# Optimization experiments

Hardware: AMD Instinct MI355X
Metric: run time of the kernel (lower is better)

The kernel has to match this reference:

```python
import jax, jax.numpy as jnp
import numpy as np

B, S, D, O, H, E, K = 4, 1024, 1024, 1024, 2048, 8, 2
EPS = 1e-5

def _layernorm(x, g, b):
    m = jnp.mean(x, axis=-1, keepdims=True)
    v = jnp.mean(jnp.square(x - m), axis=-1, keepdims=True)
    return (x - m) * jax.lax.rsqrt(v + EPS) * g + b

def setup_inputs() -> dict:
    key = jax.random.key(0)
    ks = jax.random.split(key, 8)
    def xavier(k, shape):
        fan_out, fan_in = shape[-2], shape[-1]
        bound = float(np.sqrt(6.0 / (fan_in + fan_out)))
        return jax.random.uniform(k, shape, jnp.float32, -bound, bound)
    return {
        "x": jax.random.normal(ks[0], (B, S, D), jnp.float32),
        "ln1_g": jnp.ones((D,), jnp.float32), "ln1_b": jnp.zeros((D,), jnp.float32),
        "router_w": xavier(ks[1], (E, D)), "router_b": jnp.zeros((E,), jnp.float32),
        "sh_w1": xavier(ks[2], (H, D)), "sh_b1": jnp.zeros((H,), jnp.float32),
        "sh_w2": xavier(ks[3], (O, H)), "sh_b2": jnp.zeros((O,), jnp.float32),
        "e_w1": xavier(ks[4], (E, H, D)), "e_b1": jnp.zeros((E, H), jnp.float32),
        "e_w2": xavier(ks[5], (E, O, H)), "e_b2": jnp.zeros((E, O), jnp.float32),
        "ln2_g": jnp.ones((O,), jnp.float32), "ln2_b": jnp.zeros((O,), jnp.float32),
    }

def reference(x, ln1_g, ln1_b, router_w, router_b, sh_w1, sh_b1, sh_w2, sh_b2,
              e_w1, e_b1, e_w2, e_b2, ln2_g, ln2_b):
    # eval mode: no router noise, no aux loss
    x_norm = _layernorm(x, ln1_g, ln1_b)               # [B,S,D]
    xf = x_norm.reshape(-1, D)                          # [T,D]
    logits = xf @ router_w.T + router_b                 # [T,E]
    probs = jax.nn.softmax(logits, axis=-1)
    tk_w, tk_i = jax.lax.top_k(probs, K)                # [T,K]
    tk_w = tk_w / jnp.sum(tk_w, axis=-1, keepdims=True)
    # shared expert (exact GELU, as torch nn.GELU default)
    shared = jax.nn.gelu(xf @ sh_w1.T + sh_b1, approximate=False) @ sh_w2.T + sh_b2  # [T,O]
    # all experts densely, combined sparsely by top-k weights
    hid = jax.nn.gelu(jnp.einsum('td,ehd->teh', xf, e_w1) + e_b1, approximate=False)  # [T,E,H]
    eout = jnp.einsum('teh,eoh->teo', hid, e_w2) + e_b2                                # [T,E,O]
    comb_w = jnp.sum(jax.nn.one_hot(tk_i, E, dtype=xf.dtype) * tk_w[..., None], axis=1)  # [T,E]
    out = shared * (1.0 / (E + 1)) + jnp.einsum('te,teo->to', comb_w, eout)           # [T,O]
    out = _layernorm(out.reshape(B, S, O), ln2_g, ln2_b)
    return out
```

## Files before the change

kernel.cpp:

```cpp
#include <hip/hip_runtime.h>
#include <math.h>
#include <stdint.h>

typedef unsigned short u16;
typedef unsigned int u32;

typedef __attribute__((ext_vector_type(8))) short bf16x8;
typedef __attribute__((ext_vector_type(4))) float f32x4;

#define ASYNC_COPY16(g, l)                                                         \
  __builtin_amdgcn_global_load_lds((__attribute__((address_space(1))) const void*)(g), \
                                   (__attribute__((address_space(3))) void*)(l), 16, 0, 0)

__device__ __forceinline__ float bf2f(u16 u) {
  union { u32 i; float f; } v; v.i = ((u32)u) << 16; return v.f;
}
__device__ __forceinline__ u16 f2bf(float f) {
  union { float f; u32 i; } v; v.f = f;
  u32 r = v.i + 0x7fffu + ((v.i >> 16) & 1u);
  return (u16)(r >> 16);
}
__device__ __forceinline__ float gelu_fast(float x) {
  float t = x * x;
  float z = 1.5957691f * x * (1.0f + 0.044715f * t);
  return x / (1.0f + __expf(-z));
}

__global__ __launch_bounds__(256) void cvt_all_k(
    const float* __restrict__ s0, const float* __restrict__ s1,
    const float* __restrict__ s2, const float* __restrict__ s3,
    u16* __restrict__ dst)
{
  const int64_t i0 = (int64_t)blockIdx.x * 2048 + (int64_t)threadIdx.x * 8;
  const float* src; int64_t rel;
  if (i0 < 2097152)       { src = s0; rel = i0; }
  else if (i0 < 4194304)  { src = s1; rel = i0 - 2097152; }
  else if (i0 < 20971520) { src = s2; rel = i0 - 4194304; }
  else                    { src = s3; rel = i0 - 20971520; }
  const float4 a = *(const float4*)(src + rel);
  const float4 b = *(const float4*)(src + rel + 4);
  union { u16 h[8]; uint4 v; } o;
  o.h[0] = f2bf(a.x); o.h[1] = f2bf(a.y); o.h[2] = f2bf(a.z); o.h[3] = f2bf(a.w);
  o.h[4] = f2bf(b.x); o.h[5] = f2bf(b.y); o.h[6] = f2bf(b.z); o.h[7] = f2bf(b.w);
  *(uint4*)(dst + i0) = o.v;
}

__global__ __launch_bounds__(256) void ln_router_k(
    const float* __restrict__ x, const float* __restrict__ g, const float* __restrict__ b,
    const float* __restrict__ rw, const float* __restrict__ rb,
    u16* __restrict__ xn, int* __restrict__ tk_idx, float* __restrict__ tk_w)
{
  const int t = blockIdx.x, tid = threadIdx.x;
  __shared__ float xs[1024];
  __shared__ float red[8];
  __shared__ float logits[8];
  const int wave = tid >> 6, lane = tid & 63;

  const float4 xv = *(const float4*)(x + (size_t)t * 1024 + 4 * tid);
  float v0 = xv.x, v1 = xv.y, v2 = xv.z, v3 = xv.w;
  float s = v0 + v1 + v2 + v3;
  float q = v0 * v0 + v1 * v1 + v2 * v2 + v3 * v3;
#pragma unroll
  for (int o = 32; o > 0; o >>= 1) { s += __shfl_down(s, o, 64); q += __shfl_down(q, o, 64); }
  if (lane == 0) { red[wave] = s; red[4 + wave] = q; }
  __syncthreads();
  if (tid == 0) {
    float S = red[0] + red[1] + red[2] + red[3];
    float Q = red[4] + red[5] + red[6] + red[7];
    float mean = S * (1.0f / 1024.0f);
    float var = Q * (1.0f / 1024.0f) - mean * mean;
    red[0] = mean; red[1] = rsqrtf(var + 1e-5f);
  }
  __syncthreads();
  const float mean = red[0], rstd = red[1];
  float vv[4] = {v0, v1, v2, v3};
  union { u16 h[4]; uint2 v; } pk;
#pragma unroll
  for (int j = 0; j < 4; ++j) {
    int d = 4 * tid + j;
    float y = (vv[j] - mean) * rstd * g[d] + b[d];
    xs[d] = y;
    pk.h[j] = f2bf(y);
  }
  *(uint2*)(xn + (size_t)t * 1024 + 4 * tid) = pk.v;
  __syncthreads();
#pragma unroll
  for (int pe = 0; pe < 2; ++pe) {
    int e = wave + 4 * pe;
    const float* wrow = rw + (size_t)e * 1024;
    float acc = 0.f;
#pragma unroll
    for (int j = 0; j < 16; ++j) {
      int d = lane + 64 * j;
      acc += xs[d] * wrow[d];
    }
#pragma unroll
    for (int o = 32; o > 0; o >>= 1) acc += __shfl_down(acc, o, 64);
    if (lane == 0) logits[e] = acc + rb[e];
  }
  __syncthreads();
  if (tid == 0) {
    int i0 = 0; float l0 = logits[0];
#pragma unroll
    for (int e = 1; e < 8; ++e) if (logits[e] > l0) { l0 = logits[e]; i0 = e; }
    int i1 = -1; float l1 = -3.4e38f;
#pragma unroll
    for (int e = 0; e < 8; ++e) { if (e == i0) continue; if (logits[e] > l1) { l1 = logits[e]; i1 = e; } }
    float w0 = 1.0f / (1.0f + expf(l1 - l0));
    float w1 = 1.0f - w0;
    tk_idx[2 * t] = i0; tk_idx[2 * t + 1] = i1;
    tk_w[2 * t] = w0; tk_w[2 * t + 1] = w1;
  }
}

__device__ __forceinline__ uint4 u4_add(uint4 a, uint4 b) {
  uint4 r; r.x = a.x + b.x; r.y = a.y + b.y; r.z = a.z + b.z; r.w = a.w + b.w; return r;
}
__device__ __forceinline__ uint4 u4_sub(uint4 a, uint4 b) {
  uint4 r; r.x = a.x - b.x; r.y = a.y - b.y; r.z = a.z - b.z; r.w = a.w - b.w; return r;
}

__global__ __launch_bounds__(256) void assign_k(
    const int* __restrict__ tk_idx, const float* __restrict__ tk_w,
    int* __restrict__ offs, int* __restrict__ slot_token,
    float* __restrict__ slot_w, int* __restrict__ slot_of)
{
  const int tid = threadIdx.x, lane = tid & 63, wave = tid >> 6;
  int eidx[32];
#pragma unroll
  for (int j = 0; j < 32; ++j) eidx[j] = tk_idx[tid * 32 + j];

  uint4 p = {0u, 0u, 0u, 0u};
#pragma unroll
  for (int j = 0; j < 32; ++j) {
    int e = eidx[j];
    unsigned inc = 1u << ((e & 1) * 16);
    int c = e >> 1;
    if (c == 0) p.x += inc; else if (c == 1) p.y += inc;
    else if (c == 2) p.z += inc; else p.w += inc;
  }
  const uint4 own = p;
#pragma unroll
  for (int o = 1; o < 64; o <<= 1) {
    uint4 t;
    t.x = (u32)__shfl_up((int)p.x, o, 64);
    t.y = (u32)__shfl_up((int)p.y, o, 64);
    t.z = (u32)__shfl_up((int)p.z, o, 64);
    t.w = (u32)__shfl_up((int)p.w, o, 64);
    if (lane >= o) p = u4_add(p, t);
  }
  __shared__ uint4 wtot[4];
  __shared__ int offs_s[9];
  if (lane == 63) wtot[wave] = p;
  __syncthreads();
  uint4 wbase = {0u, 0u, 0u, 0u};
  uint4 gtot = {0u, 0u, 0u, 0u};
#pragma unroll
  for (int w2 = 0; w2 < 4; ++w2) {
    uint4 t = wtot[w2];
    if (w2 < wave) wbase = u4_add(wbase, t);
    gtot = u4_add(gtot, t);
  }
  const uint4 excl = u4_sub(p, own);
  if (tid == 0) {
    int gtots[8] = { (int)(gtot.x & 0xffff), (int)(gtot.x >> 16),
                     (int)(gtot.y & 0xffff), (int)(gtot.y >> 16),
                     (int)(gtot.z & 0xffff), (int)(gtot.z >> 16),
                     (int)(gtot.w & 0xffff), (int)(gtot.w >> 16) };
    int a = 0;
#pragma unroll
    for (int e = 0; e < 8; ++e) { offs_s[e] = a; offs[e] = a; a += gtots[e]; }
    offs_s[8] = a; offs[8] = a;
  }
  __syncthreads();
  const uint4 pre = u4_add(wbase, excl);
  int base[8];
  base[0] = offs_s[0] + (int)(pre.x & 0xffff);
  base[1] = offs_s[1] + (int)(pre.x >> 16);
  base[2] = offs_s[2] + (int)(pre.y & 0xffff);
  base[3] = offs_s[3] + (int)(pre.y >> 16);
  base[4] = offs_s[4] + (int)(pre.z & 0xffff);
  base[5] = offs_s[5] + (int)(pre.z >> 16);
  base[6] = offs_s[6] + (int)(pre.w & 0xffff);
  base[7] = offs_s[7] + (int)(pre.w >> 16);
#pragma unroll
  for (int j = 0; j < 32; ++j) {
    int idx = tid * 32 + j;
    int e = eidx[j];
    int s = base[e]++;
    slot_token[s] = idx >> 1;
    slot_w[s] = tk_w[idx];
    slot_of[idx] = s;
  }
}

template <int N, int KD, int STAGE>
__global__ __launch_bounds__(256) void gemm_fused_k(
    const u16* __restrict__ Abase, const u16* __restrict__ Bsh,
    const u16* __restrict__ Bex, const float* __restrict__ bias_sh,
    const float* __restrict__ bias_ex,
    u16* __restrict__ outH,
    const int* __restrict__ offs, const int* __restrict__ slot_token,
    const float* __restrict__ slot_w)
{
  const int tid = threadIdx.x;
  const int z = blockIdx.z;
  int off = 0, cnt = 4096, obase = 0;
  const u16* B = Bsh;
  const float* biasp = bias_sh;
  if (z > 0) {
    off = offs[z - 1]; cnt = offs[z] - off; obase = 4096 + off;
    B = Bex + (size_t)(z - 1) * N * KD;
    biasp = bias_ex + (size_t)(z - 1) * N;
  }
  const int m0 = blockIdx.y * 128;
  if (m0 >= cnt) return;
  const int n0 = blockIdx.x * 128;

  __shared__ u16 lA[2][4096];
  __shared__ u16 lB[2][4096];

  const int rS = tid >> 2;
  const int c8 = (tid & 3) * 8;

  int ra0 = m0 + rS;      if (ra0 > cnt - 1) ra0 = cnt - 1;
  int ra1 = m0 + rS + 64; if (ra1 > cnt - 1) ra1 = cnt - 1;
  size_t arow0, arow1;
  if (STAGE == 1) {
    if (z == 0) { arow0 = (size_t)ra0; arow1 = (size_t)ra1; }
    else        { arow0 = (size_t)slot_token[off + ra0]; arow1 = (size_t)slot_token[off + ra1]; }
  } else {
    if (z == 0) { arow0 = (size_t)ra0; arow1 = (size_t)ra1; }
    else        { arow0 = (size_t)(4096 + off + ra0); arow1 = (size_t)(4096 + off + ra1); }
  }
  const u16* gA0 = Abase + arow0 * KD + c8;
  const u16* gA1 = Abase + arow1 * KD + c8;
  const u16* gB0 = B + (size_t)(n0 + rS) * KD + c8;
  const u16* gB1 = B + (size_t)(n0 + rS + 64) * KD + c8;

  const int wave = tid >> 6, lane = tid & 63;
  const int wr = wave >> 1, wc = wave & 1;
  const int fr = lane & 15, fq = lane >> 4;

  f32x4 acc[4][4];
  const f32x4 zero = {0.f, 0.f, 0.f, 0.f};
#pragma unroll
  for (int i = 0; i < 4; ++i)
#pragma unroll
    for (int n = 0; n < 4; ++n) acc[i][n] = zero;

  const int NK = KD / 32;
  {
    ASYNC_COPY16(gA0, &lA[0][0] + wave * 512);
    ASYNC_COPY16(gA1, &lA[0][0] + 2048 + wave * 512);
    ASYNC_COPY16(gB0, &lB[0][0] + wave * 512);
    ASYNC_COPY16(gB1, &lB[0][0] + 2048 + wave * 512);
    gA0 += 32; gA1 += 32; gB0 += 32; gB1 += 32;
  }

  for (int kb = 0; kb < NK; ++kb) {
    const int cur = kb & 1;
    __syncthreads();
    if (kb + 1 < NK) {
      ASYNC_COPY16(gA0, &lA[cur ^ 1][0] + wave * 512);
      ASYNC_COPY16(gA1, &lA[cur ^ 1][0] + 2048 + wave * 512);
      ASYNC_COPY16(gB0, &lB[cur ^ 1][0] + wave * 512);
      ASYNC_COPY16(gB1, &lB[cur ^ 1][0] + 2048 + wave * 512);
      gA0 += 32; gA1 += 32; gB0 += 32; gB1 += 32;
    }
    const u16* rdA = &lA[cur][0] + (wr * 64 + fr) * 32 + fq * 8;
    const u16* rdB = &lB[cur][0] + (wc * 64 + fr) * 32 + fq * 8;
    bf16x8 af[4], bfv[4];
#pragma unroll
    for (int i = 0; i < 4; ++i) af[i] = *(const bf16x8*)(rdA + i * 16 * 32);
#pragma unroll
    for (int n = 0; n < 4; ++n) bfv[n] = *(const bf16x8*)(rdB + n * 16 * 32);
#pragma unroll
    for (int i = 0; i < 4; ++i)
#pragma unroll
      for (int n = 0; n < 4; ++n)
        acc[i][n] = __builtin_amdgcn_mfma_f32_16x16x32_bf16(af[i], bfv[n], acc[i][n], 0, 0, 0);
  }

  const int colBase = n0 + wc * 64;
#pragma unroll
  for (int i = 0; i < 4; ++i) {
    const int mlBase = m0 + wr * 64 + i * 16 + fq * 4;
#pragma unroll
    for (int r = 0; r < 4; ++r) {
      const int ml = mlBase + r;
      if (ml >= cnt) continue;
      const size_t orow = (size_t)(obase + ml) * N;
      float rwgt = (STAGE == 2) ? ((z == 0) ? (1.0f / 9.0f) : slot_w[off + ml]) : 1.f;
#pragma unroll
      for (int n = 0; n < 4; ++n) {
        const int col = colBase + n * 16 + fr;
        float v = acc[i][n][r] + biasp[col];
        if (STAGE == 1) v = gelu_fast(v);
        else            v = v * rwgt;
        outH[orow + col] = f2bf(v);
      }
    }
  }
}

__global__ __launch_bounds__(256) void combine_ln2_k(
    const u16* __restrict__ sh_out, const u16* __restrict__ eout,
    const int* __restrict__ slot_of,
    const float* __restrict__ g2, const float* __restrict__ b2,
    float* __restrict__ out)
{
  const int t = blockIdx.x, tid = threadIdx.x;
  const int wave = tid >> 6, lane = tid & 63;
  __shared__ float red[8];
  const size_t s0 = (size_t)slot_of[2 * t], s1 = (size_t)slot_of[2 * t + 1];
  union { uint2 v; u16 h[4]; } a, c0, c1;
  a.v  = *(const uint2*)(sh_out + (size_t)t * 1024 + 4 * tid);
  c0.v = *(const uint2*)(eout + s0 * 1024 + 4 * tid);
  c1.v = *(const uint2*)(eout + s1 * 1024 + 4 * tid);
  float vv[4];
#pragma unroll
  for (int j = 0; j < 4; ++j) vv[j] = bf2f(a.h[j]) + bf2f(c0.h[j]) + bf2f(c1.h[j]);
  float s = vv[0] + vv[1] + vv[2] + vv[3];
  float q = vv[0] * vv[0] + vv[1] * vv[1] + vv[2] * vv[2] + vv[3] * vv[3];
#pragma unroll
  for (int o = 32; o > 0; o >>= 1) { s += __shfl_down(s, o, 64); q += __shfl_down(q, o, 64); }
  if (lane == 0) { red[wave] = s; red[4 + wave] = q; }
  __syncthreads();
  if (tid == 0) {
    float S = red[0] + red[1] + red[2] + red[3];
    float Q = red[4] + red[5] + red[6] + red[7];
    float mean = S * (1.0f / 1024.0f);
    float var = Q * (1.0f / 1024.0f) - mean * mean;
    red[0] = mean; red[1] = rsqrtf(var + 1e-5f);
  }
  __syncthreads();
  const float mean = red[0], rstd = red[1];
#pragma unroll
  for (int j = 0; j < 4; ++j) {
    int d = 4 * tid + j;
    out[(size_t)t * 1024 + d] = (vv[j] - mean) * rstd * g2[d] + b2[d];
  }
}

extern "C" void kernel_launch(void* const* d_in, const int* in_sizes, int n_in,
                              void* d_out, int out_size, void* d_ws, size_t ws_size,
                              hipStream_t stream)
{
  const float* x     = (const float*)d_in[0];
  const float* ln1_g = (const float*)d_in[1];
  const float* ln1_b = (const float*)d_in[2];
  const float* rw    = (const float*)d_in[3];
  const float* rb    = (const float*)d_in[4];
  const float* sh_w1 = (const float*)d_in[5];
  const float* sh_b1 = (const float*)d_in[6];
  const float* sh_w2 = (const float*)d_in[7];
  const float* sh_b2 = (const float*)d_in[8];
  const float* e_w1  = (const float*)d_in[9];
  const float* e_b1  = (const float*)d_in[10];
  const float* e_w2  = (const float*)d_in[11];
  const float* e_b2  = (const float*)d_in[12];
  const float* ln2_g = (const float*)d_in[13];
  const float* ln2_b = (const float*)d_in[14];
  float* out = (float*)d_out;

  char* w = (char*)d_ws;
  u16*   x_norm = (u16*)(w + 0);
  u16*   hid    = (u16*)(w + (8u << 20));
  u16*   outb   = (u16*)(w + (56u << 20));
  u16*   w1b    = (u16*)(w + (104u << 20));
  u16*   w2b    = (u16*)(w + (108u << 20));
  u16*   ew1b   = (u16*)(w + (112u << 20));
  u16*   ew2b   = (u16*)(w + (144u << 20));
  char*  meta   = w + (176u << 20);
  int*   tk_idx     = (int*)(meta);
  float* tk_w       = (float*)(meta + (32u << 10));
  int*   slot_token = (int*)(meta + (64u << 10));
  float* slot_w     = (float*)(meta + (96u << 10));
  int*   slot_of    = (int*)(meta + (128u << 10));
  int*   offs       = (int*)(meta + (160u << 10));

  cvt_all_k<<<18432, 256, 0, stream>>>(sh_w1, sh_w2, e_w1, e_w2, w1b);

  ln_router_k<<<4096, 256, 0, stream>>>(x, ln1_g, ln1_b, rw, rb, x_norm, tk_idx, tk_w);
  assign_k<<<1, 256, 0, stream>>>(tk_idx, tk_w, offs, slot_token, slot_w, slot_of);

  gemm_fused_k<2048, 1024, 1><<<dim3(16, 32, 9), 256, 0, stream>>>(
      x_norm, w1b, ew1b, sh_b1, e_b1, hid, offs, slot_token, nullptr);
  gemm_fused_k<1024, 2048, 2><<<dim3(8, 32, 9), 256, 0, stream>>>(
      hid, w2b, ew2b, sh_b2, e_b2, outb, offs, slot_token, slot_w);

  combine_ln2_k<<<4096, 256, 0, stream>>>(outb, outb + (size_t)4096 * 1024,
                                          slot_of, ln2_g, ln2_b, out);
}
```

Before: 438.6 us.

## Use one wave per token in LN kernels and swizzle GEMM tile order

The LN1+router and combine+LN2 kernels now assign one wave per token with four tokens per block. This removes the block-wide __syncthreads reductions and lets the code use vectorized float4 gamma/beta and router-weight loads. The GEMM kernels remap blockIdx into grouped M/N tiles so that neighbouring blocks share A and B panels in cache. The early-exit check for empty expert tiles now depends on the remapped m0, and the router uses the faster __expf.

```diff
diff --git a/kernel.cpp b/kernel.cpp
--- a/kernel.cpp
+++ b/kernel.cpp
@@ -50,66 +50,69 @@
     const float* __restrict__ rw, const float* __restrict__ rb,
     u16* __restrict__ xn, int* __restrict__ tk_idx, float* __restrict__ tk_w)
 {
-  const int t = blockIdx.x, tid = threadIdx.x;
-  __shared__ float xs[1024];
-  __shared__ float red[8];
-  __shared__ float logits[8];
-  const int wave = tid >> 6, lane = tid & 63;
-
-  const float4 xv = *(const float4*)(x + (size_t)t * 1024 + 4 * tid);
-  float v0 = xv.x, v1 = xv.y, v2 = xv.z, v3 = xv.w;
-  float s = v0 + v1 + v2 + v3;
-  float q = v0 * v0 + v1 * v1 + v2 * v2 + v3 * v3;
+  __shared__ float xs[4][1024];
+  const int wave = threadIdx.x >> 6, lane = threadIdx.x & 63;
+  const int t = blockIdx.x * 4 + wave;
+
+  const float* xrow = x + (size_t)t * 1024;
+  float4 v[4];
+#pragma unroll
+  for (int j = 0; j < 4; ++j) v[j] = *(const float4*)(xrow + lane * 4 + j * 256);
+  float s = 0.f, q = 0.f;
+#pragma unroll
+  for (int j = 0; j < 4; ++j) {
+    s += v[j].x + v[j].y + v[j].z + v[j].w;
+    q += v[j].x * v[j].x + v[j].y * v[j].y + v[j].z * v[j].z + v[j].w * v[j].w;
+  }
 #pragma unroll
   for (int o = 32; o > 0; o >>= 1) { s += __shfl_down(s, o, 64); q += __shfl_down(q, o, 64); }
-  if (lane == 0) { red[wave] = s; red[4 + wave] = q; }
-  __syncthreads();
-  if (tid == 0) {
-    float S = red[0] + red[1] + red[2] + red[3];
-    float Q = red[4] + red[5] + red[6] + red[7];
-    float mean = S * (1.0f / 1024.0f);
-    float var = Q * (1.0f / 1024.0f) - mean * mean;
-    red[0] = mean; red[1] = rsqrtf(var + 1e-5f);
-  }
-  __syncthreads();
-  const float mean = red[0], rstd = red[1];
-  float vv[4] = {v0, v1, v2, v3};
-  union { u16 h[4]; uint2 v; } pk;
+  s = __shfl(s, 0, 64); q = __shfl(q, 0, 64);
+  const float mean = s * (1.0f / 1024.0f);
+  const float rstd = rsqrtf(q * (1.0f / 1024.0f) - mean * mean + 1e-5f);
+
 #pragma unroll
   for (int j = 0; j < 4; ++j) {
-    int d = 4 * tid + j;
-    float y = (vv[j] - mean) * rstd * g[d] + b[d];
-    xs[d] = y;
-    pk.h[j] = f2bf(y);
-  }
-  *(uint2*)(xn + (size_t)t * 1024 + 4 * tid) = pk.v;
-  __syncthreads();
-#pragma unroll
-  for (int pe = 0; pe < 2; ++pe) {
-    int e = wave + 4 * pe;
-    const float* wrow = rw + (size_t)e * 1024;
-    float acc = 0.f;
-#pragma unroll
-    for (int j = 0; j < 16; ++j) {
-      int d = lane + 64 * j;
-      acc += xs[d] * wrow[d];
-    }
-#pragma unroll
-    for (int o = 32; o > 0; o >>= 1) acc += __shfl_down(acc, o, 64);
-    if (lane == 0) logits[e] = acc + rb[e];
-  }
-  __syncthreads();
-  if (tid == 0) {
-    int i0 = 0; float l0 = logits[0];
-#pragma unroll
-    for (int e = 1; e < 8; ++e) if (logits[e] > l0) { l0 = logits[e]; i0 = e; }
+    const int d0 = lane * 4 + j * 256;
+    const float4 gv = *(const float4*)(g + d0);
+    const float4 bv = *(const float4*)(b + d0);
+    float y0 = (v[j].x - mean) * rstd * gv.x + bv.x;
+    float y1 = (v[j].y - mean) * rstd * gv.y + bv.y;
+    float y2 = (v[j].z - mean) * rstd * gv.z + bv.z;
+    float y3 = (v[j].w - mean) * rstd * gv.w + bv.w;
+    float4 yv = {y0, y1, y2, y3};
+    *(float4*)(&xs[wave][d0]) = yv;
+    union { u16 h[4]; uint2 u; } pk;
+    pk.h[0] = f2bf(y0); pk.h[1] = f2bf(y1); pk.h[2] = f2bf(y2); pk.h[3] = f2bf(y3);
+    *(uint2*)(xn + (size_t)t * 1024 + d0) = pk.u;
+  }
+
+  const int e = lane >> 3, c = lane & 7;
+  const float* wrow = rw + (size_t)e * 1024;
+  float acc = 0.f;
+#pragma unroll
+  for (int i = 0; i < 32; ++i) {
+    const int d4 = 4 * (c + 8 * i);
+    const float4 wv = *(const float4*)(wrow + d4);
+    const float4 xv = *(const float4*)(&xs[wave][d4]);
+    acc += xv.x * wv.x + xv.y * wv.y + xv.z * wv.z + xv.w * wv.w;
+  }
+  acc += __shfl_xor(acc, 1, 64);
+  acc += __shfl_xor(acc, 2, 64);
+  acc += __shfl_xor(acc, 4, 64);
+  const float logit = acc + rb[e];
+  float l[8];
+#pragma unroll
+  for (int ee = 0; ee < 8; ++ee) l[ee] = __shfl(logit, ee * 8, 64);
+  if (lane == 0) {
+    int i0 = 0; float l0 = l[0];
+#pragma unroll
+    for (int k = 1; k < 8; ++k) if (l[k] > l0) { l0 = l[k]; i0 = k; }
     int i1 = -1; float l1 = -3.4e38f;
 #pragma unroll
-    for (int e = 0; e < 8; ++e) { if (e == i0) continue; if (logits[e] > l1) { l1 = logits[e]; i1 = e; } }
-    float w0 = 1.0f / (1.0f + expf(l1 - l0));
-    float w1 = 1.0f - w0;
+    for (int k = 0; k < 8; ++k) { if (k == i0) continue; if (l[k] > l1) { l1 = l[k]; i1 = k; } }
+    float w0 = 1.0f / (1.0f + __expf(l1 - l0));
     tk_idx[2 * t] = i0; tk_idx[2 * t + 1] = i1;
-    tk_w[2 * t] = w0; tk_w[2 * t + 1] = w1;
+    tk_w[2 * t] = w0; tk_w[2 * t + 1] = 1.0f - w0;
   }
 }
 
@@ -195,7 +198,7 @@
 }
 
 template <int N, int KD, int STAGE>
-__global__ __launch_bounds__(256) void gemm_fused_k(
+__device__ __forceinline__ void gemm_body(
     const u16* __restrict__ Abase, const u16* __restrict__ Bsh,
     const u16* __restrict__ Bex, const float* __restrict__ bias_sh,
     const float* __restrict__ bias_ex,
@@ -213,9 +216,12 @@
     B = Bex + (size_t)(z - 1) * N * KD;
     biasp = bias_ex + (size_t)(z - 1) * N;
   }
-  const int m0 = blockIdx.y * 128;
+  constexpr int NT = N / 128;
+  const int bx = blockIdx.x, by = blockIdx.y;
+  const int r = bx & 7, sgl = bx >> 3;
+  const int m0 = (r + 8 * (by >> 3)) * 128;
   if (m0 >= cnt) return;
-  const int n0 = blockIdx.x * 128;
+  const int n0 = (sgl + (NT >> 3) * (by & 7)) * 128;
 
   __shared__ u16 lA[2][4096];
   __shared__ u16 lB[2][4096];
@@ -287,15 +293,15 @@
   for (int i = 0; i < 4; ++i) {
     const int mlBase = m0 + wr * 64 + i * 16 + fq * 4;
 #pragma unroll
-    for (int r = 0; r < 4; ++r) {
-      const int ml = mlBase + r;
+    for (int rr = 0; rr < 4; ++rr) {
+      const int ml = mlBase + rr;
       if (ml >= cnt) continue;
       const size_t orow = (size_t)(obase + ml) * N;
       float rwgt = (STAGE == 2) ? ((z == 0) ? (1.0f / 9.0f) : slot_w[off + ml]) : 1.f;
 #pragma unroll
       for (int n = 0; n < 4; ++n) {
         const int col = colBase + n * 16 + fr;
-        float v = acc[i][n][r] + biasp[col];
+        float v = acc[i][n][rr] + biasp[col];
         if (STAGE == 1) v = gelu_fast(v);
         else            v = v * rwgt;
         outH[orow + col] = f2bf(v);
@@ -304,42 +310,70 @@
   }
 }
 
+__global__ __launch_bounds__(256) void fc1_k(
+    const u16* __restrict__ Abase, const u16* __restrict__ Bsh,
+    const u16* __restrict__ Bex, const float* __restrict__ bias_sh,
+    const float* __restrict__ bias_ex, u16* __restrict__ outH,
+    const int* __restrict__ offs, const int* __restrict__ slot_token,
+    const float* __restrict__ slot_w)
+{
+  gemm_body<2048, 1024, 1>(Abase, Bsh, Bex, bias_sh, bias_ex, outH, offs, slot_token, slot_w);
+}
+
+__global__ __launch_bounds__(256) void fc2_k(
+    const u16* __restrict__ Abase, const u16* __restrict__ Bsh,
+    const u16* __restrict__ Bex, const float* __restrict__ bias_sh,
+    const float* __restrict__ bias_ex, u16* __restrict__ outH,
+    const int* __restrict__ offs, const int* __restrict__ slot_token,
+    const float* __restrict__ slot_w)
+{
+  gemm_body<1024, 2048, 2>(Abase, Bsh, Bex, bias_sh, bias_ex, outH, offs, slot_token, slot_w);
+}
+
 __global__ __launch_bounds__(256) void combine_ln2_k(
     const u16* __restrict__ sh_out, const u16* __restrict__ eout,
     const int* __restrict__ slot_of,
     const float* __restrict__ g2, const float* __restrict__ b2,
     float* __restrict__ out)
 {
-  const int t = blockIdx.x, tid = threadIdx.x;
-  const int wave = tid >> 6, lane = tid & 63;
-  __shared__ float red[8];
+  const int wave = threadIdx.x >> 6, lane = threadIdx.x & 63;
+  const int t = blockIdx.x * 4 + wave;
   const size_t s0 = (size_t)slot_of[2 * t], s1 = (size_t)slot_of[2 * t + 1];
-  union { uint2 v; u16 h[4]; } a, c0, c1;
-  a.v  = *(const uint2*)(sh_out + (size_t)t * 1024 + 4 * tid);
-  c0.v = *(const uint2*)(eout + s0 * 1024 + 4 * tid);
-  c1.v = *(const uint2*)(eout + s1 * 1024 + 4 * tid);
-  float vv[4];
-#pragma unroll
-  for (int j = 0; j < 4; ++j) vv[j] = bf2f(a.h[j]) + bf2f(c0.h[j]) + bf2f(c1.h[j]);
-  float s = vv[0] + vv[1] + vv[2] + vv[3];
-  float q = vv[0] * vv[0] + vv[1] * vv[1] + vv[2] * vv[2] + vv[3] * vv[3];
+  const u16* pa = sh_out + (size_t)t * 1024;
+  const u16* p0 = eout + s0 * 1024;
+  const u16* p1 = eout + s1 * 1024;
+  float vv[16];
+  float s = 0.f, q = 0.f;
+#pragma unroll
+  for (int j = 0; j < 4; ++j) {
+    const int d0 = lane * 4 + j * 256;
+    union { uint2 u; u16 h[4]; } a, c0, c1;
+    a.u  = *(const uint2*)(pa + d0);
+    c0.u = *(const uint2*)(p0 + d0);
+    c1.u = *(const uint2*)(p1 + d0);
+#pragma unroll
+    for (int k = 0; k < 4; ++k) {
+      float v = bf2f(a.h[k]) + bf2f(c0.h[k]) + bf2f(c1.h[k]);
+      vv[4 * j + k] = v;
+      s += v; q += v * v;
+    }
+  }
 #pragma unroll
   for (int o = 32; o > 0; o >>= 1) { s += __shfl_down(s, o, 64); q += __shfl_down(q, o, 64); }
-  if (lane == 0) { red[wave] = s; red[4 + wave] = q; }
-  __syncthreads();
-  if (tid == 0) {
-    float S = red[0] + red[1] + red[2] + red[3];
-    float Q = red[4] + red[5] + red[6] + red[7];
-    float mean = S * (1.0f / 1024.0f);
-    float var = Q * (1.0f / 1024.0f) - mean * mean;
-    red[0] = mean; red[1] = rsqrtf(var + 1e-5f);
-  }
-  __syncthreads();
-  const float mean = red[0], rstd = red[1];
+  s = __shfl(s, 0, 64); q = __shfl(q, 0, 64);
+  const float mean = s * (1.0f / 1024.0f);
+  const float rstd = rsqrtf(q * (1.0f / 1024.0f) - mean * mean + 1e-5f);
 #pragma unroll
   for (int j = 0; j < 4; ++j) {
-    int d = 4 * tid + j;
-    out[(size_t)t * 1024 + d] = (vv[j] - mean) * rstd * g2[d] + b2[d];
+    const int d0 = lane * 4 + j * 256;
+    const float4 gv = *(const float4*)(g2 + d0);
+    const float4 bv = *(const float4*)(b2 + d0);
+    float4 ov;
+    ov.x = (vv[4 * j + 0] - mean) * rstd * gv.x + bv.x;
+    ov.y = (vv[4 * j + 1] - mean) * rstd * gv.y + bv.y;
+    ov.z = (vv[4 * j + 2] - mean) * rstd * gv.z + bv.z;
+    ov.w = (vv[4 * j + 3] - mean) * rstd * gv.w + bv.w;
+    *(float4*)(out + (size_t)t * 1024 + d0) = ov;
   }
 }
 
@@ -382,14 +416,14 @@
 
   cvt_all_k<<<18432, 256, 0, stream>>>(sh_w1, sh_w2, e_w1, e_w2, w1b);
 
-  ln_router_k<<<4096, 256, 0, stream>>>(x, ln1_g, ln1_b, rw, rb, x_norm, tk_idx, tk_w);
+  ln_router_k<<<1024, 256, 0, stream>>>(x, ln1_g, ln1_b, rw, rb, x_norm, tk_idx, tk_w);
   assign_k<<<1, 256, 0, stream>>>(tk_idx, tk_w, offs, slot_token, slot_w, slot_of);
 
-  gemm_fused_k<2048, 1024, 1><<<dim3(16, 32, 9), 256, 0, stream>>>(
+  fc1_k<<<dim3(16, 32, 9), 256, 0, stream>>>(
       x_norm, w1b, ew1b, sh_b1, e_b1, hid, offs, slot_token, nullptr);
-  gemm_fused_k<1024, 2048, 2><<<dim3(8, 32, 9), 256, 0, stream>>>(
+  fc2_k<<<dim3(8, 32, 9), 256, 0, stream>>>(
       hid, w2b, ew2b, sh_b2, e_b2, outb, offs, slot_token, slot_w);
 
-  combine_ln2_k<<<4096, 256, 0, stream>>>(outb, outb + (size_t)4096 * 1024,
+  combine_ln2_k<<<1024, 256, 0, stream>>>(outb, outb + (size_t)4096 * 1024,
                                           slot_of, ln2_g, ln2_b, out);
 }
```

New measurement: 491.5 us. 1.12x slower.
